# Optimization experiments

Hardware: AMD Instinct MI355X
Metric: run time of the kernel (lower is better)

The kernel has to match this reference:

```python
import jax, jax.numpy as jnp
import numpy as np

D, N, L, H, VOCAB = 256, 8192, 6, 4, 256
EPS = 1e-5


def layernorm(x):
    # LayerNorm over last dim, no affine (matches nn.LayerNorm(D, elementwise_affine=False))
    mu = jnp.mean(x, axis=-1, keepdims=True)
    var = jnp.mean(jnp.square(x - mu), axis=-1, keepdims=True)
    return (x - mu) * jax.lax.rsqrt(var + EPS)


def rotate_half(x):
    x1, x2 = jnp.split(x, 2, axis=-1)
    return jnp.concatenate((-x2, x1), axis=-1)


def rope_tables(T, dim, dtype):
    inv_freq = 1.0 / (10000.0 ** (jnp.arange(0, dim, 2, dtype=jnp.float32) / dim))
    t = jnp.arange(T, dtype=jnp.float32)
    freqs = jnp.einsum('i,j->ij', t, inv_freq)          # [T, dim/2]
    emb = jnp.concatenate((freqs, freqs), axis=-1)       # [T, dim]
    return jnp.cos(emb).astype(dtype), jnp.sin(emb).astype(dtype)


def linear_attention(Q, K, V):
    # unnormalized causal attention with RoPE on Q, K
    B, T, d = Q.shape
    cos, sin = rope_tables(T, d, Q.dtype)
    Qr = Q * cos + rotate_half(Q) * sin
    Kr = K * cos + rotate_half(K) * sin
    energy = jnp.einsum('btd,bsd->bts', Qr, Kr)          # [B, T, T]
    mask = jnp.tril(jnp.ones((T, T), dtype=energy.dtype))
    energy = energy * mask
    return jnp.einsum('bts,bsd->btd', energy, V)


def setup_inputs() -> dict:
    key = jax.random.key(0)
    ks = jax.random.split(key, 6)
    idx = jax.random.randint(ks[0], (4, 2048), 0, VOCAB)
    wte = jax.random.normal(ks[1], (VOCAB, D), dtype=jnp.float32) * 0.02
    encoder = jax.random.normal(ks[2], (N, D), dtype=jnp.float32) * 0.02
    decoder_x = jax.random.normal(ks[3], (H, D, N // H), dtype=jnp.float32) * 0.02
    decoder_y = jax.random.normal(ks[4], (H, D, N // H), dtype=jnp.float32) * 0.02
    readout = jax.random.normal(ks[5], (D, VOCAB), dtype=jnp.float32) * 0.02
    return {"idx": idx, "wte": wte, "encoder": encoder,
            "decoder_x": decoder_x, "decoder_y": decoder_y, "readout": readout}


def reference(idx, wte, encoder, decoder_x, decoder_y, readout):
    B, T = idx.shape
    v_ast = layernorm(wte[idx])                          # [B, T, D]
    for _ in range(L):
        x_raw = jnp.einsum('btd,hdm->bthm', v_ast, decoder_x)
        x = jax.nn.relu(x_raw)                           # [B, T, H, N/H]
        a_ast = linear_attention(v_ast, v_ast, v_ast)
        y_raw = jnp.einsum('btd,hdm->bthm', layernorm(a_ast), decoder_y)
        y = jax.nn.relu(y_raw) * x
        y_flat = y.reshape(B, T, -1)                     # [B, T, N]
        update = y_flat @ encoder                        # [B, T, D]
        v_ast = v_ast + layernorm(update)
    logits = v_ast @ readout                             # [B, T, VOCAB]
    return logits
```

## Files before the change

kernel.cpp:

```cpp
#include <hip/hip_runtime.h>
#include <hip/hip_bf16.h>

typedef __hip_bfloat16 bf16;
typedef _Float16 half_t;
typedef __attribute__((ext_vector_type(8))) _Float16 half8;
typedef __attribute__((ext_vector_type(4))) float f32x4;

#define LN_EPS 1e-5f

static constexpr int Dk     = 256;
static constexpr int Tk     = 2048;
static constexpr int BTk    = 8192;
static constexpr int MHk    = 2048;
static constexpr int Nk     = 8192;
static constexpr int LAYERS = 6;
static constexpr long long TD  = (long long)Tk * Dk;
static constexpr long long BTD = (long long)BTk * Dk;
static constexpr long long TT  = (long long)Tk * Tk;

#define SKQ(t) ((((t) & 3) ^ (((t) >> 3) & 3)) * 8)

__device__ __forceinline__ float wave_reduce(float v) {
#pragma unroll
    for (int o = 32; o > 0; o >>= 1) v += __shfl_down(v, o);
    return v;
}

__device__ __forceinline__ float block_sum_256(float x, float* sbuf) {
    float s = wave_reduce(x);
    int lane = threadIdx.x & 63, wv = threadIdx.x >> 6;
    if (lane == 0) sbuf[wv] = s;
    __syncthreads();
    float r = sbuf[0] + sbuf[1] + sbuf[2] + sbuf[3];
    __syncthreads();
    return r;
}

__device__ __forceinline__ void glds16(const void* g, void* lds) {
    __builtin_amdgcn_global_load_lds(
        (const __attribute__((address_space(1))) void*)g,
        (__attribute__((address_space(3))) void*)lds, 16, 0, 0);
}

__device__ __forceinline__ void rope_row(const float* nv, int t, half_t* qrow) {
    int i = threadIdx.x;
    if (i < 128) {
        float invf = powf(10000.f, -(float)i / 128.f);
        float ang = (float)t * invf;
        float s, c;
        sincosf(ang, &s, &c);
        float q1 = nv[i], q2 = nv[128 + i];
        qrow[i]       = (half_t)(q1 * c - q2 * s);
        qrow[128 + i] = (half_t)(q2 * c + q1 * s);
    }
}

__global__ __launch_bounds__(256) void sniff_kernel(const unsigned short* __restrict__ w,
                                                    int* __restrict__ flag) {
    __shared__ float sbuf[4];
    int tid = threadIdx.x;
    float cnt = 0.f;
    for (int i = tid; i < 1024; i += 256) {
        int e = (w[i] >> 7) & 0xFF;
        if (e >= 128) cnt += 1.f;
    }
    float tot = block_sum_256(cnt, sbuf);
    if (tid == 0) *flag = (tot > 32.f) ? 1 : 0;
}

__global__ __launch_bounds__(256) void tr_cvt16_kernel(const void* __restrict__ src,
                                                       const int* __restrict__ flag,
                                                       half_t* __restrict__ dst,
                                                       int R, int C,
                                                       long long sz, long long dz) {
    __shared__ float t[32][33];
    bool f32 = (*flag != 0);
    int ct = blockIdx.x * 32, rt = blockIdx.y * 32;
    long long so = (long long)blockIdx.z * sz, dofs = (long long)blockIdx.z * dz;
    int tx = threadIdx.x & 31, ty = threadIdx.x >> 5;
#pragma unroll
    for (int i = 0; i < 4; i++) {
        long long idx = so + (long long)(rt + ty + i * 8) * C + ct + tx;
        t[ty + i * 8][tx] = f32 ? ((const float*)src)[idx] : (float)((const bf16*)src)[idx];
    }
    __syncthreads();
#pragma unroll
    for (int i = 0; i < 4; i++) {
        long long odx = dofs + (long long)(ct + ty + i * 8) * R + rt + tx;
        dst[odx] = (half_t)t[tx][ty + i * 8];
    }
}

__global__ __launch_bounds__(256) void trv_kernel(const float* __restrict__ src,
                                                  half_t* __restrict__ dst) {
    __shared__ float t[32][33];
    int ct = blockIdx.x * 32, rt = blockIdx.y * 32;
    int tx = threadIdx.x & 31, ty = threadIdx.x >> 5;
#pragma unroll
    for (int i = 0; i < 4; i++)
        t[ty + i * 8][tx] = src[(long long)(rt + ty + i * 8) * Dk + ct + tx];
    __syncthreads();
#pragma unroll
    for (int i = 0; i < 4; i++)
        dst[(long long)(ct + ty + i * 8) * BTk + rt + tx] = (half_t)t[tx][ty + i * 8];
}

__global__ __launch_bounds__(256) void embed_ln_kernel(const int* __restrict__ idx,
                                                       const void* __restrict__ wte,
                                                       const int* __restrict__ flag,
                                                       float* __restrict__ v,
                                                       half_t* __restrict__ vf,
                                                       half_t* __restrict__ qf) {
    __shared__ float sbuf[4];
    __shared__ float nvs[256];
    int bt = blockIdx.x, tid = threadIdx.x;
    int id = idx[bt];
    bool f32 = (*flag != 0);
    float x = f32 ? ((const float*)wte)[id * Dk + tid]
                  : (float)((const bf16*)wte)[id * Dk + tid];
    float mu = block_sum_256(x, sbuf) * (1.f / 256.f);
    float d = x - mu;
    float var = block_sum_256(d * d, sbuf) * (1.f / 256.f);
    float r = d * rsqrtf(var + LN_EPS);
    v[bt * Dk + tid] = r;
    vf[bt * Dk + tid] = (half_t)r;
    nvs[tid] = r;
    __syncthreads();
    rope_row(nvs, bt & (Tk - 1), qf + (long long)bt * Dk);
}

__global__ __launch_bounds__(256) void ln_rows_kernel(const float* __restrict__ Pa,
                                                      half_t* __restrict__ of) {
    __shared__ float sbuf[4];
    int bt = blockIdx.x, tid = threadIdx.x;
    int b = bt >> 11, t = bt & (Tk - 1);
    int ncnt = ((t & ~127) >> 9) + 1;
    const float* p = Pa + ((long long)(b << 2)) * TD + (long long)t * Dk + tid;
    float x = 0.f;
    for (int c = 0; c < ncnt; c++) x += p[(long long)c * TD];
    float mu = block_sum_256(x, sbuf) * (1.f / 256.f);
    float d = x - mu;
    float var = block_sum_256(d * d, sbuf) * (1.f / 256.f);
    float r = d * rsqrtf(var + LN_EPS);
    of[bt * Dk + tid] = (half_t)r;
}

__global__ __launch_bounds__(256) void add_ln_kernel(const float* __restrict__ Pu,
                                                     float* __restrict__ v,
                                                     half_t* __restrict__ vf,
                                                     half_t* __restrict__ qf) {
    __shared__ float sbuf[4];
    __shared__ float nvs[256];
    int bt = blockIdx.x, tid = threadIdx.x;
    long long e = (long long)bt * Dk + tid;
    float x = Pu[e] + Pu[e + BTD] + Pu[e + 2 * BTD] + Pu[e + 3 * BTD];
    float mu = block_sum_256(x, sbuf) * (1.f / 256.f);
    float d = x - mu;
    float var = block_sum_256(d * d, sbuf) * (1.f / 256.f);
    float r = d * rsqrtf(var + LN_EPS);
    float nv = v[e] + r;
    v[e] = nv;
    vf[e] = (half_t)nv;
    nvs[tid] = nv;
    __syncthreads();
    rope_row(nvs, bt & (Tk - 1), qf + (long long)bt * Dk);
}

__global__ __launch_bounds__(256) void gemm128e(
    const half_t* __restrict__ Q, half_t* __restrict__ E) {
    __shared__ __align__(16) half_t As[128 * 32];
    __shared__ __align__(16) half_t Bs[128 * 32];
    const int tid = threadIdx.x;
    const int lane = tid & 63, wv = tid >> 6;
    const int wr = wv >> 1, wc = wv & 1;
    const int quad = lane >> 4, r = lane & 15;
    const int qsw = (quad ^ ((r >> 1) & 3)) * 8;
    const int mb = blockIdx.y * 128, nb = blockIdx.x * 128;
    if ((int)blockIdx.x > (int)blockIdx.y) return;
    const half_t* Qb = Q + (long long)blockIdx.z * TD;
    half_t* Eb = E + (long long)blockIdx.z * TT;

    f32x4 acc[4][4] = {};
    const int srow = tid >> 2, skq = SKQ(tid);
    const int wbase = (tid & 192) * 8;
    for (int k0 = 0; k0 < Dk; k0 += 32) {
#pragma unroll
        for (int rnd = 0; rnd < 2; rnd++) {
            int row = rnd * 64 + srow;
            glds16(Qb + (long long)(mb + row) * Dk + k0 + skq, As + rnd * 2048 + wbase);
            glds16(Qb + (long long)(nb + row) * Dk + k0 + skq, Bs + rnd * 2048 + wbase);
        }
        __syncthreads();
        half8 bfr[4];
#pragma unroll
        for (int ni = 0; ni < 4; ni++)
            bfr[ni] = *(const half8*)&Bs[(wc * 64 + ni * 16 + r) * 32 + qsw];
#pragma unroll
        for (int mi = 0; mi < 4; mi++) {
            half8 afr = *(const half8*)&As[(wr * 64 + mi * 16 + r) * 32 + qsw];
#pragma unroll
            for (int ni = 0; ni < 4; ni++)
                acc[mi][ni] = __builtin_amdgcn_mfma_f32_16x16x32_f16(afr, bfr[ni], acc[mi][ni], 0, 0, 0);
        }
        __syncthreads();
    }
#pragma unroll
    for (int mi = 0; mi < 4; mi++)
#pragma unroll
        for (int ni = 0; ni < 4; ni++) {
            int row0 = mb + wr * 64 + mi * 16 + quad * 4;
            int col = nb + wc * 64 + ni * 16 + r;
#pragma unroll
            for (int rr = 0; rr < 4; rr++) {
                int row = row0 + rr;
                float val = (row < col) ? 0.f : acc[mi][ni][rr];
                Eb[(long long)row * Tk + col] = (half_t)val;
            }
        }
}

__global__ __launch_bounds__(256) void gemm128a(
    const half_t* __restrict__ E, const half_t* __restrict__ vT,
    float* __restrict__ Pa) {
    __shared__ __align__(16) half_t As[128 * 32];
    __shared__ __align__(16) half_t Bs[128 * 32];
    const int tid = threadIdx.x;
    const int lane = tid & 63, wv = tid >> 6;
    const int wr = wv >> 1, wc = wv & 1;
    const int quad = lane >> 4, r = lane & 15;
    const int qsw = (quad ^ ((r >> 1) & 3)) * 8;
    const int mb = blockIdx.x * 128, nb = blockIdx.y * 128;
    const int b = blockIdx.z >> 2, c = blockIdx.z & 3;
    const int kbeg = c * 512;
    const int kend = min(mb + 128, kbeg + 512);
    if (kend <= kbeg) return;

    const half_t* Ab = E + (long long)b * TT;
    const half_t* Bb = vT + (long long)b * Tk;
    float* Pc = Pa + (long long)blockIdx.z * TD;
    f32x4 acc[4][4] = {};
    const int srow = tid >> 2, skq = SKQ(tid);
    const int wbase = (tid & 192) * 8;
    for (int k0 = kbeg; k0 < kend; k0 += 32) {
#pragma unroll
        for (int rnd = 0; rnd < 2; rnd++) {
            int row = rnd * 64 + srow;
            glds16(Ab + (long long)(mb + row) * Tk + k0 + skq, As + rnd * 2048 + wbase);
            glds16(Bb + (long long)(nb + row) * BTk + k0 + skq, Bs + rnd * 2048 + wbase);
        }
        __syncthreads();
        half8 bfr[4];
#pragma unroll
        for (int ni = 0; ni < 4; ni++)
            bfr[ni] = *(const half8*)&Bs[(wc * 64 + ni * 16 + r) * 32 + qsw];
#pragma unroll
        for (int mi = 0; mi < 4; mi++) {
            half8 afr = *(const half8*)&As[(wr * 64 + mi * 16 + r) * 32 + qsw];
#pragma unroll
            for (int ni = 0; ni < 4; ni++)
                acc[mi][ni] = __builtin_amdgcn_mfma_f32_16x16x32_f16(afr, bfr[ni], acc[mi][ni], 0, 0, 0);
        }
        __syncthreads();
    }
#pragma unroll
    for (int mi = 0; mi < 4; mi++)
#pragma unroll
        for (int ni = 0; ni < 4; ni++) {
            int row0 = mb + wr * 64 + mi * 16 + quad * 4;
            int col = nb + wc * 64 + ni * 16 + r;
#pragma unroll
            for (int rr = 0; rr < 4; rr++)
                Pc[(long long)(row0 + rr) * Dk + col] = acc[mi][ni][rr];
        }
}

__global__ __launch_bounds__(256, 2) void dual_gemm(
    const half_t* __restrict__ A1,
    const half_t* __restrict__ A2,
    const half_t* __restrict__ dxT,
    const half_t* __restrict__ dyT,
    half_t* __restrict__ C) {
    __shared__ __align__(16) half_t As1[128 * 64];
    __shared__ __align__(16) half_t As2[128 * 64];
    __shared__ __align__(16) half_t Bs1[128 * 64];
    __shared__ __align__(16) half_t Bs2[128 * 64];
    const int tid = threadIdx.x;
    const int lane = tid & 63, wv = tid >> 6;
    const int wr = wv >> 1, wc = wv & 1;
    const int quad = lane >> 4, r = lane & 15;
    const int flat = blockIdx.x + 16 * (blockIdx.y + 64 * blockIdx.z);
    const int xcd = flat & 7, j = flat >> 3;
    const int mt = (xcd >> 2) * 32 + (j >> 4);
    const int nt = (xcd & 3) * 4 + (j & 3);
    const int h  = (j >> 2) & 3;
    const int mb = mt * 128, nb = nt * 128;
    const half_t* B1 = dxT + (long long)h * MHk * Dk;
    const half_t* B2 = dyT + (long long)h * MHk * Dk;

    f32x4 accX[4][4] = {};
    f32x4 accY[4][4] = {};
    const int srow8 = lane >> 3;
    const int soct  = (lane & 7) ^ srow8;
    for (int k0 = 0; k0 < Dk; k0 += 64) {
#pragma unroll
        for (int c = 0; c < 4; c++) {
            int row = wv * 32 + c * 8;
            long long ga = (long long)(mb + row + srow8) * Dk + k0 + soct * 8;
            long long gb = (long long)(nb + row + srow8) * Dk + k0 + soct * 8;
            glds16(A1 + ga, As1 + row * 64);
            glds16(A2 + ga, As2 + row * 64);
            glds16(B1 + gb, Bs1 + row * 64);
            glds16(B2 + gb, Bs2 + row * 64);
        }
        __syncthreads();
#pragma unroll
        for (int sub = 0; sub < 2; sub++) {
            half8 b1f[4], b2f[4];
#pragma unroll
            for (int ni = 0; ni < 4; ni++) {
                int R = wc * 64 + ni * 16 + r;
                int pos = ((sub * 4 + quad) ^ (R & 7)) * 8;
                b1f[ni] = *(const half8*)&Bs1[R * 64 + pos];
                b2f[ni] = *(const half8*)&Bs2[R * 64 + pos];
            }
#pragma unroll
            for (int mi = 0; mi < 4; mi++) {
                int R = wr * 64 + mi * 16 + r;
                int pos = ((sub * 4 + quad) ^ (R & 7)) * 8;
                half8 a1 = *(const half8*)&As1[R * 64 + pos];
                half8 a2 = *(const half8*)&As2[R * 64 + pos];
#pragma unroll
                for (int ni = 0; ni < 4; ni++) {
                    accX[mi][ni] = __builtin_amdgcn_mfma_f32_16x16x32_f16(a1, b1f[ni], accX[mi][ni], 0, 0, 0);
                    accY[mi][ni] = __builtin_amdgcn_mfma_f32_16x16x32_f16(a2, b2f[ni], accY[mi][ni], 0, 0, 0);
                }
            }
        }
        __syncthreads();
    }
#pragma unroll
    for (int mi = 0; mi < 4; mi++)
#pragma unroll
        for (int ni = 0; ni < 4; ni++) {
            int row0 = mb + wr * 64 + mi * 16 + quad * 4;
            int col = h * MHk + nb + wc * 64 + ni * 16 + r;
#pragma unroll
            for (int rr = 0; rr < 4; rr++) {
                float val = fmaxf(accY[mi][ni][rr], 0.f) * fmaxf(accX[mi][ni][rr], 0.f);
                C[(long long)(row0 + rr) * Nk + col] = (half_t)val;
            }
        }
}

__global__ __launch_bounds__(256) void gemm128u(
    const half_t* __restrict__ A, const half_t* __restrict__ B,
    float* __restrict__ Pu) {
    __shared__ __align__(16) half_t As[128 * 32];
    __shared__ __align__(16) half_t Bs[128 * 32];
    const int tid = threadIdx.x;
    const int lane = tid & 63, wv = tid >> 6;
    const int wr = wv >> 1, wc = wv & 1;
    const int quad = lane >> 4, r = lane & 15;
    const int qsw = (quad ^ ((r >> 1) & 3)) * 8;
    const int mb = blockIdx.x * 128, nb = blockIdx.y * 128;
    const int kbeg = blockIdx.z * 2048;
    float* Pc = Pu + (long long)blockIdx.z * BTD;

    f32x4 acc[4][4] = {};
    const int srow = tid >> 2, skq = SKQ(tid);
    const int wbase = (tid & 192) * 8;
    for (int k0 = kbeg; k0 < kbeg + 2048; k0 += 32) {
#pragma unroll
        for (int rnd = 0; rnd < 2; rnd++) {
            int row = rnd * 64 + srow;
            glds16(A + (long long)(mb + row) * Nk + k0 + skq, As + rnd * 2048 + wbase);
            glds16(B + (long long)(nb + row) * Nk + k0 + skq, Bs + rnd * 2048 + wbase);
        }
        __syncthreads();
        half8 bfr[4];
#pragma unroll
        for (int ni = 0; ni < 4; ni++)
            bfr[ni] = *(const half8*)&Bs[(wc * 64 + ni * 16 + r) * 32 + qsw];
#pragma unroll
        for (int mi = 0; mi < 4; mi++) {
            half8 afr = *(const half8*)&As[(wr * 64 + mi * 16 + r) * 32 + qsw];
#pragma unroll
            for (int ni = 0; ni < 4; ni++)
                acc[mi][ni] = __builtin_amdgcn_mfma_f32_16x16x32_f16(afr, bfr[ni], acc[mi][ni], 0, 0, 0);
        }
        __syncthreads();
    }
#pragma unroll
    for (int mi = 0; mi < 4; mi++)
#pragma unroll
        for (int ni = 0; ni < 4; ni++) {
            int row0 = mb + wr * 64 + mi * 16 + quad * 4;
            int col = nb + wc * 64 + ni * 16 + r;
#pragma unroll
            for (int rr = 0; rr < 4; rr++)
                Pc[(long long)(row0 + rr) * Dk + col] = acc[mi][ni][rr];
        }
}

__global__ __launch_bounds__(256) void gemm64h(
    const half_t* __restrict__ A, int lda,
    const half_t* __restrict__ B, int ldb,
    float* __restrict__ C, int ldc, int K) {
    __shared__ __align__(16) half_t As[64 * 32];
    __shared__ __align__(16) half_t Bs[64 * 32];
    const int tid = threadIdx.x;
    const int lane = tid & 63, wv = tid >> 6;
    const int wr = wv >> 1, wc = wv & 1;
    const int quad = lane >> 4, r = lane & 15;
    const int qsw = (quad ^ ((r >> 1) & 3)) * 8;
    const int mb = blockIdx.y * 64, nb = blockIdx.x * 64;

    f32x4 acc[2][2] = {};
    const int srow = tid >> 2, skq = SKQ(tid);
    const int wbase = (tid & 192) * 8;
    for (int k0 = 0; k0 < K; k0 += 32) {
        glds16(A + (long long)(mb + srow) * lda + k0 + skq, As + wbase);
        glds16(B + (long long)(nb + srow) * ldb + k0 + skq, Bs + wbase);
        __syncthreads();
        half8 b0 = *(const half8*)&Bs[(wc * 32 +  0 + r) * 32 + qsw];
        half8 b1 = *(const half8*)&Bs[(wc * 32 + 16 + r) * 32 + qsw];
#pragma unroll
        for (int mi = 0; mi < 2; mi++) {
            half8 afr = *(const half8*)&As[(wr * 32 + mi * 16 + r) * 32 + qsw];
            acc[mi][0] = __builtin_amdgcn_mfma_f32_16x16x32_f16(afr, b0, acc[mi][0], 0, 0, 0);
            acc[mi][1] = __builtin_amdgcn_mfma_f32_16x16x32_f16(afr, b1, acc[mi][1], 0, 0, 0);
        }
        __syncthreads();
    }
#pragma unroll
    for (int mi = 0; mi < 2; mi++)
#pragma unroll
        for (int ni = 0; ni < 2; ni++) {
            int row0 = mb + wr * 32 + mi * 16 + quad * 4;
            int col = nb + wc * 32 + ni * 16 + r;
#pragma unroll
            for (int rr = 0; rr < 4; rr++)
                C[(long long)(row0 + rr) * ldc + col] = acc[mi][ni][rr];
        }
}

extern "C" void kernel_launch(void* const* d_in, const int* in_sizes, int n_in,
                              void* d_out, int out_size, void* d_ws, size_t ws_size,
                              hipStream_t stream) {
    (void)in_sizes; (void)n_in; (void)out_size; (void)ws_size;
    const int* idx = (const int*)d_in[0];
    float* out = (float*)d_out;

    char* ws = (char*)d_ws;
    float*  v32  = (float*) (ws);
    half_t* vf   = (half_t*)(ws + (  8ll << 20));
    half_t* qf   = (half_t*)(ws + ( 12ll << 20));
    half_t* vT   = (half_t*)(ws + ( 16ll << 20));
    half_t* lnf  = (half_t*)(ws + ( 20ll << 20));
    half_t* E    = (half_t*)(ws + ( 24ll << 20));
    float*  Pa   = (float*) (ws + ( 56ll << 20));
    float*  Pu   = (float*) (ws + ( 24ll << 20));
    half_t* y16  = (half_t*)(ws + ( 88ll << 20));
    half_t* dxT  = (half_t*)(ws + (216ll << 20));
    half_t* dyT  = (half_t*)(ws + (220ll << 20));
    half_t* eT   = (half_t*)(ws + (224ll << 20));
    half_t* roT  = (half_t*)(ws + (228ll << 20));
    int*    flag = (int*)   (ws + (228ll << 20) + (256ll << 10));

    sniff_kernel<<<1, 256, 0, stream>>>((const unsigned short*)d_in[1], flag);
    tr_cvt16_kernel<<<dim3(MHk / 32, Dk / 32, 4), 256, 0, stream>>>(
        d_in[3], flag, dxT, Dk, MHk, (long long)Dk * MHk, (long long)Dk * MHk);
    tr_cvt16_kernel<<<dim3(MHk / 32, Dk / 32, 4), 256, 0, stream>>>(
        d_in[4], flag, dyT, Dk, MHk, (long long)Dk * MHk, (long long)Dk * MHk);
    tr_cvt16_kernel<<<dim3(Dk / 32, Nk / 32, 1), 256, 0, stream>>>(
        d_in[2], flag, eT, Nk, Dk, 0, 0);
    tr_cvt16_kernel<<<dim3(Dk / 32, Dk / 32, 1), 256, 0, stream>>>(
        d_in[5], flag, roT, Dk, Dk, 0, 0);

    embed_ln_kernel<<<BTk, 256, 0, stream>>>(idx, d_in[1], flag, v32, vf, qf);

    for (int l = 0; l < LAYERS; l++) {
        trv_kernel<<<dim3(Dk / 32, BTk / 32), 256, 0, stream>>>(v32, vT);
        gemm128e<<<dim3(Tk / 128, Tk / 128, 4), 256, 0, stream>>>(qf, E);
        gemm128a<<<dim3(Tk / 128, Dk / 128, 16), 256, 0, stream>>>(E, vT, Pa);
        ln_rows_kernel<<<BTk, 256, 0, stream>>>(Pa, lnf);
        dual_gemm<<<dim3(MHk / 128, BTk / 128, 4), 256, 0, stream>>>(
            vf, lnf, dxT, dyT, y16);
        gemm128u<<<dim3(BTk / 128, Dk / 128, 4), 256, 0, stream>>>(y16, eT, Pu);
        add_ln_kernel<<<BTk, 256, 0, stream>>>(Pu, v32, vf, qf);
    }
    gemm64h<<<dim3(Dk / 64, BTk / 64), 256, 0, stream>>>(
        vf, Dk, roT, Dk, out, Dk, Dk);
}
```

Measured before the change: 1.281 ms.

## Fuse dual decoder GEMM with encoder GEMM, keeping y tiles in LDS

Merges the dual decoder GEMM (relu(x)*relu(y)) and the encoder projection into one kernel. Each block owns 128 rows and one head and loops over 16 column tiles of that head. Each y tile is written to LDS and immediately multiplied against the matching slice of the encoder, accumulating into a 128x256 register tile. This removes the round trip of the 8192x8192 fp16 y intermediate through global memory and drops one launch. In exchange there are only 256 blocks at occupancy 1, more accumulator registers per thread and serialized phases, so latency hiding and parallelism may suffer.

```diff
diff --git a/kernel.cpp b/kernel.cpp
--- a/kernel.cpp
+++ b/kernel.cpp
@@ -274,131 +274,135 @@
         }
 }
 
-__global__ __launch_bounds__(256, 2) void dual_gemm(
+__global__ __launch_bounds__(256, 1) void dual_update(
     const half_t* __restrict__ A1,
     const half_t* __restrict__ A2,
     const half_t* __restrict__ dxT,
     const half_t* __restrict__ dyT,
-    half_t* __restrict__ C) {
-    __shared__ __align__(16) half_t As1[128 * 64];
-    __shared__ __align__(16) half_t As2[128 * 64];
-    __shared__ __align__(16) half_t Bs1[128 * 64];
-    __shared__ __align__(16) half_t Bs2[128 * 64];
-    const int tid = threadIdx.x;
-    const int lane = tid & 63, wv = tid >> 6;
-    const int wr = wv >> 1, wc = wv & 1;
-    const int quad = lane >> 4, r = lane & 15;
-    const int flat = blockIdx.x + 16 * (blockIdx.y + 64 * blockIdx.z);
-    const int xcd = flat & 7, j = flat >> 3;
-    const int mt = (xcd >> 2) * 32 + (j >> 4);
-    const int nt = (xcd & 3) * 4 + (j & 3);
-    const int h  = (j >> 2) & 3;
-    const int mb = mt * 128, nb = nt * 128;
-    const half_t* B1 = dxT + (long long)h * MHk * Dk;
-    const half_t* B2 = dyT + (long long)h * MHk * Dk;
-
-    f32x4 accX[4][4] = {};
-    f32x4 accY[4][4] = {};
-    const int srow8 = lane >> 3;
-    const int soct  = (lane & 7) ^ srow8;
-    for (int k0 = 0; k0 < Dk; k0 += 64) {
-#pragma unroll
-        for (int c = 0; c < 4; c++) {
-            int row = wv * 32 + c * 8;
-            long long ga = (long long)(mb + row + srow8) * Dk + k0 + soct * 8;
-            long long gb = (long long)(nb + row + srow8) * Dk + k0 + soct * 8;
-            glds16(A1 + ga, As1 + row * 64);
-            glds16(A2 + ga, As2 + row * 64);
-            glds16(B1 + gb, Bs1 + row * 64);
-            glds16(B2 + gb, Bs2 + row * 64);
-        }
-        __syncthreads();
-#pragma unroll
-        for (int sub = 0; sub < 2; sub++) {
-            half8 b1f[4], b2f[4];
-#pragma unroll
-            for (int ni = 0; ni < 4; ni++) {
-                int R = wc * 64 + ni * 16 + r;
-                int pos = ((sub * 4 + quad) ^ (R & 7)) * 8;
-                b1f[ni] = *(const half8*)&Bs1[R * 64 + pos];
-                b2f[ni] = *(const half8*)&Bs2[R * 64 + pos];
-            }
-#pragma unroll
-            for (int mi = 0; mi < 4; mi++) {
-                int R = wr * 64 + mi * 16 + r;
-                int pos = ((sub * 4 + quad) ^ (R & 7)) * 8;
-                half8 a1 = *(const half8*)&As1[R * 64 + pos];
-                half8 a2 = *(const half8*)&As2[R * 64 + pos];
-#pragma unroll
-                for (int ni = 0; ni < 4; ni++) {
-                    accX[mi][ni] = __builtin_amdgcn_mfma_f32_16x16x32_f16(a1, b1f[ni], accX[mi][ni], 0, 0, 0);
-                    accY[mi][ni] = __builtin_amdgcn_mfma_f32_16x16x32_f16(a2, b2f[ni], accY[mi][ni], 0, 0, 0);
-                }
-            }
-        }
-        __syncthreads();
-    }
-#pragma unroll
-    for (int mi = 0; mi < 4; mi++)
-#pragma unroll
-        for (int ni = 0; ni < 4; ni++) {
-            int row0 = mb + wr * 64 + mi * 16 + quad * 4;
-            int col = h * MHk + nb + wc * 64 + ni * 16 + r;
-#pragma unroll
-            for (int rr = 0; rr < 4; rr++) {
-                float val = fmaxf(accY[mi][ni][rr], 0.f) * fmaxf(accX[mi][ni][rr], 0.f);
-                C[(long long)(row0 + rr) * Nk + col] = (half_t)val;
-            }
-        }
-}
-
-__global__ __launch_bounds__(256) void gemm128u(
-    const half_t* __restrict__ A, const half_t* __restrict__ B,
+    const half_t* __restrict__ eT,
     float* __restrict__ Pu) {
-    __shared__ __align__(16) half_t As[128 * 32];
-    __shared__ __align__(16) half_t Bs[128 * 32];
+    __shared__ __align__(16) half_t smem[32768];
+    half_t* As1 = smem;
+    half_t* As2 = smem + 8192;
+    half_t* Bs1 = smem + 16384;
+    half_t* Bs2 = smem + 24576;
+    half_t* yld = smem;
+    half_t* eTs = smem + 16384;
+
     const int tid = threadIdx.x;
     const int lane = tid & 63, wv = tid >> 6;
     const int wr = wv >> 1, wc = wv & 1;
     const int quad = lane >> 4, r = lane & 15;
     const int qsw = (quad ^ ((r >> 1) & 3)) * 8;
-    const int mb = blockIdx.x * 128, nb = blockIdx.y * 128;
-    const int kbeg = blockIdx.z * 2048;
-    float* Pc = Pu + (long long)blockIdx.z * BTD;
-
-    f32x4 acc[4][4] = {};
+    const int xcd = blockIdx.x & 7, j = blockIdx.x >> 3;
+    const int mt = xcd * 8 + (j & 7);
+    const int h = j >> 3;
+    const int mb = mt * 128;
+    const half_t* B1 = dxT + (long long)h * MHk * Dk;
+    const half_t* B2 = dyT + (long long)h * MHk * Dk;
+    const half_t* Eh = eT + (long long)h * MHk;
+    float* Pc = Pu + (long long)h * BTD;
+
+    const int srow8 = lane >> 3;
+    const int soct  = (lane & 7) ^ srow8;
     const int srow = tid >> 2, skq = SKQ(tid);
     const int wbase = (tid & 192) * 8;
-    for (int k0 = kbeg; k0 < kbeg + 2048; k0 += 32) {
-#pragma unroll
-        for (int rnd = 0; rnd < 2; rnd++) {
+
+    f32x4 accU[4][8] = {};
+    for (int nt = 0; nt < 16; ++nt) {
+        const int nb = nt * 128;
+        f32x4 accX[4][4] = {};
+        f32x4 accY[4][4] = {};
+        for (int k0 = 0; k0 < Dk; k0 += 64) {
+#pragma unroll
+            for (int st = 0; st < 4; st++) {
+                int row = wv * 32 + st * 8;
+                long long ga = (long long)(mb + row + srow8) * Dk + k0 + soct * 8;
+                long long gb = (long long)(nb + row + srow8) * Dk + k0 + soct * 8;
+                glds16(A1 + ga, As1 + row * 64);
+                glds16(A2 + ga, As2 + row * 64);
+                glds16(B1 + gb, Bs1 + row * 64);
+                glds16(B2 + gb, Bs2 + row * 64);
+            }
+            __syncthreads();
+#pragma unroll
+            for (int sub = 0; sub < 2; sub++) {
+                half8 b1f[4], b2f[4];
+#pragma unroll
+                for (int ni = 0; ni < 4; ni++) {
+                    int R = wc * 64 + ni * 16 + r;
+                    int pos = ((sub * 4 + quad) ^ (R & 7)) * 8;
+                    b1f[ni] = *(const half8*)&Bs1[R * 64 + pos];
+                    b2f[ni] = *(const half8*)&Bs2[R * 64 + pos];
+                }
+#pragma unroll
+                for (int mi = 0; mi < 4; mi++) {
+                    int R = wr * 64 + mi * 16 + r;
+                    int pos = ((sub * 4 + quad) ^ (R & 7)) * 8;
+                    half8 a1 = *(const half8*)&As1[R * 64 + pos];
+                    half8 a2 = *(const half8*)&As2[R * 64 + pos];
+#pragma unroll
+                    for (int ni = 0; ni < 4; ni++) {
+                        accX[mi][ni] = __builtin_amdgcn_mfma_f32_16x16x32_f16(a1, b1f[ni], accX[mi][ni], 0, 0, 0);
+                        accY[mi][ni] = __builtin_amdgcn_mfma_f32_16x16x32_f16(a2, b2f[ni], accY[mi][ni], 0, 0, 0);
+                    }
+                }
+            }
+            __syncthreads();
+        }
+#pragma unroll
+        for (int mi = 0; mi < 4; mi++)
+#pragma unroll
+            for (int ni = 0; ni < 4; ni++) {
+                int col = wc * 64 + ni * 16 + r;
+                int row0 = wr * 64 + mi * 16 + quad * 4;
+#pragma unroll
+                for (int rr = 0; rr < 4; rr++) {
+                    int W = row0 + rr;
+                    float val = fmaxf(accY[mi][ni][rr], 0.f) * fmaxf(accX[mi][ni][rr], 0.f);
+                    yld[W * 128 + (((col >> 3) ^ ((W & 12) >> 1)) << 3) + (col & 7)] = (half_t)val;
+                }
+            }
+#pragma unroll
+        for (int rnd = 0; rnd < 4; rnd++) {
             int row = rnd * 64 + srow;
-            glds16(A + (long long)(mb + row) * Nk + k0 + skq, As + rnd * 2048 + wbase);
-            glds16(B + (long long)(nb + row) * Nk + k0 + skq, Bs + rnd * 2048 + wbase);
-        }
-        __syncthreads();
-        half8 bfr[4];
-#pragma unroll
-        for (int ni = 0; ni < 4; ni++)
-            bfr[ni] = *(const half8*)&Bs[(wc * 64 + ni * 16 + r) * 32 + qsw];
-#pragma unroll
-        for (int mi = 0; mi < 4; mi++) {
-            half8 afr = *(const half8*)&As[(wr * 64 + mi * 16 + r) * 32 + qsw];
-#pragma unroll
-            for (int ni = 0; ni < 4; ni++)
-                acc[mi][ni] = __builtin_amdgcn_mfma_f32_16x16x32_f16(afr, bfr[ni], acc[mi][ni], 0, 0, 0);
-        }
-        __syncthreads();
+            glds16(Eh + (long long)row * Nk + nb + skq, eTs + rnd * 2048 + wbase);
+        }
+        __syncthreads();
+#pragma unroll
+        for (int c = 0; c < 4; ++c) {
+            if (c < 3) {
+#pragma unroll
+                for (int rnd = 0; rnd < 4; rnd++) {
+                    int row = rnd * 64 + srow;
+                    glds16(Eh + (long long)row * Nk + nb + (c + 1) * 32 + skq,
+                           eTs + ((c + 1) & 1) * 8192 + rnd * 2048 + wbase);
+                }
+            }
+            half8 bu[8];
+#pragma unroll
+            for (int ni = 0; ni < 8; ni++)
+                bu[ni] = *(const half8*)&eTs[(c & 1) * 8192 + (wc * 128 + ni * 16 + r) * 32 + qsw];
+#pragma unroll
+            for (int mi = 0; mi < 4; mi++) {
+                int R = wr * 64 + mi * 16 + r;
+                half8 au = *(const half8*)&yld[R * 128 + ((((c << 2) + quad) ^ ((R & 12) >> 1)) << 3)];
+#pragma unroll
+                for (int ni = 0; ni < 8; ni++)
+                    accU[mi][ni] = __builtin_amdgcn_mfma_f32_16x16x32_f16(au, bu[ni], accU[mi][ni], 0, 0, 0);
+            }
+            __syncthreads();
+        }
     }
 #pragma unroll
     for (int mi = 0; mi < 4; mi++)
 #pragma unroll
-        for (int ni = 0; ni < 4; ni++) {
+        for (int ni = 0; ni < 8; ni++) {
             int row0 = mb + wr * 64 + mi * 16 + quad * 4;
-            int col = nb + wc * 64 + ni * 16 + r;
+            int col = wc * 128 + ni * 16 + r;
 #pragma unroll
             for (int rr = 0; rr < 4; rr++)
-                Pc[(long long)(row0 + rr) * Dk + col] = acc[mi][ni][rr];
+                Pc[(long long)(row0 + rr) * Dk + col] = accU[mi][ni][rr];
         }
 }
 
@@ -460,7 +464,6 @@
     half_t* E    = (half_t*)(ws + ( 24ll << 20));
     float*  Pa   = (float*) (ws + ( 56ll << 20));
     float*  Pu   = (float*) (ws + ( 24ll << 20));
-    half_t* y16  = (half_t*)(ws + ( 88ll << 20));
     half_t* dxT  = (half_t*)(ws + (216ll << 20));
     half_t* dyT  = (half_t*)(ws + (220ll << 20));
     half_t* eT   = (half_t*)(ws + (224ll << 20));
@@ -484,9 +487,7 @@
         gemm128e<<<dim3(Tk / 128, Tk / 128, 4), 256, 0, stream>>>(qf, E);
         gemm128a<<<dim3(Tk / 128, Dk / 128, 16), 256, 0, stream>>>(E, vT, Pa);
         ln_rows_kernel<<<BTk, 256, 0, stream>>>(Pa, lnf);
-        dual_gemm<<<dim3(MHk / 128, BTk / 128, 4), 256, 0, stream>>>(
-            vf, lnf, dxT, dyT, y16);
-        gemm128u<<<dim3(BTk / 128, Dk / 128, 4), 256, 0, stream>>>(y16, eT, Pu);
+        dual_update<<<dim3(256), 256, 0, stream>>>(vf, lnf, dxT, dyT, eT, Pu);
         add_ln_kernel<<<BTk, 256, 0, stream>>>(Pu, v32, vf, qf);
     }
     gemm64h<<<dim3(Dk / 64, BTk / 64), 256, 0, stream>>>(
```

New measurement: 1.527 ms. +19.2%, slower.

## Double-buffer LDS staging in dual_gemm and gemm128u with wave priority boost

Applied to the files above, without the earlier changes.

Both the dual projection GEMM and the split-K encoder GEMM now use two LDS buffers. The global-to-LDS loads for the next K step are issued before the MFMA work on the current buffer, so each iteration needs one barrier instead of two. dual_gemm also switches from a 64-wide K tile to a 32-wide one so the double buffer fits in the same LDS budget. MFMA sections are wrapped in s_setprio, and gemm128u gets a launch bound of 2 blocks per CU. The cost is more barriers in dual_gemm (8 K steps instead of 4) and doubled LDS use in gemm128u, which could limit occupancy.

```diff
diff --git a/kernel.cpp b/kernel.cpp
--- a/kernel.cpp
+++ b/kernel.cpp
@@ -280,14 +280,15 @@
     const half_t* __restrict__ dxT,
     const half_t* __restrict__ dyT,
     half_t* __restrict__ C) {
-    __shared__ __align__(16) half_t As1[128 * 64];
-    __shared__ __align__(16) half_t As2[128 * 64];
-    __shared__ __align__(16) half_t Bs1[128 * 64];
-    __shared__ __align__(16) half_t Bs2[128 * 64];
+    __shared__ __align__(16) half_t As1[2][128 * 32];
+    __shared__ __align__(16) half_t As2[2][128 * 32];
+    __shared__ __align__(16) half_t Bs1[2][128 * 32];
+    __shared__ __align__(16) half_t Bs2[2][128 * 32];
     const int tid = threadIdx.x;
     const int lane = tid & 63, wv = tid >> 6;
     const int wr = wv >> 1, wc = wv & 1;
     const int quad = lane >> 4, r = lane & 15;
+    const int qsw = (quad ^ ((r >> 1) & 3)) * 8;
     const int flat = blockIdx.x + 16 * (blockIdx.y + 64 * blockIdx.z);
     const int xcd = flat & 7, j = flat >> 3;
     const int mt = (xcd >> 2) * 32 + (j >> 4);
@@ -299,43 +300,48 @@
 
     f32x4 accX[4][4] = {};
     f32x4 accY[4][4] = {};
-    const int srow8 = lane >> 3;
-    const int soct  = (lane & 7) ^ srow8;
-    for (int k0 = 0; k0 < Dk; k0 += 64) {
-#pragma unroll
-        for (int c = 0; c < 4; c++) {
-            int row = wv * 32 + c * 8;
-            long long ga = (long long)(mb + row + srow8) * Dk + k0 + soct * 8;
-            long long gb = (long long)(nb + row + srow8) * Dk + k0 + soct * 8;
-            glds16(A1 + ga, As1 + row * 64);
-            glds16(A2 + ga, As2 + row * 64);
-            glds16(B1 + gb, Bs1 + row * 64);
-            glds16(B2 + gb, Bs2 + row * 64);
-        }
-        __syncthreads();
-#pragma unroll
-        for (int sub = 0; sub < 2; sub++) {
-            half8 b1f[4], b2f[4];
+    const int srow = tid >> 2, skq = SKQ(tid);
+    const int wbase = (tid & 192) * 8;
+
+    auto stage = [&](int ks, int bsel) {
+        const int k0 = ks * 32;
+#pragma unroll
+        for (int rnd = 0; rnd < 2; rnd++) {
+            int row = rnd * 64 + srow;
+            long long ga = (long long)(mb + row) * Dk + k0 + skq;
+            long long gb = (long long)(nb + row) * Dk + k0 + skq;
+            glds16(A1 + ga, &As1[bsel][rnd * 2048 + wbase]);
+            glds16(A2 + ga, &As2[bsel][rnd * 2048 + wbase]);
+            glds16(B1 + gb, &Bs1[bsel][rnd * 2048 + wbase]);
+            glds16(B2 + gb, &Bs2[bsel][rnd * 2048 + wbase]);
+        }
+    };
+
+    stage(0, 0);
+    __syncthreads();
+    for (int ks = 0; ks < 8; ks++) {
+        const int cur = ks & 1;
+        if (ks < 7) stage(ks + 1, cur ^ 1);
+        __builtin_amdgcn_s_setprio(1);
+        half8 b1f[4], b2f[4];
+#pragma unroll
+        for (int ni = 0; ni < 4; ni++) {
+            int R = wc * 64 + ni * 16 + r;
+            b1f[ni] = *(const half8*)&Bs1[cur][R * 32 + qsw];
+            b2f[ni] = *(const half8*)&Bs2[cur][R * 32 + qsw];
+        }
+#pragma unroll
+        for (int mi = 0; mi < 4; mi++) {
+            int R = wr * 64 + mi * 16 + r;
+            half8 a1 = *(const half8*)&As1[cur][R * 32 + qsw];
+            half8 a2 = *(const half8*)&As2[cur][R * 32 + qsw];
 #pragma unroll
             for (int ni = 0; ni < 4; ni++) {
-                int R = wc * 64 + ni * 16 + r;
-                int pos = ((sub * 4 + quad) ^ (R & 7)) * 8;
-                b1f[ni] = *(const half8*)&Bs1[R * 64 + pos];
-                b2f[ni] = *(const half8*)&Bs2[R * 64 + pos];
+                accX[mi][ni] = __builtin_amdgcn_mfma_f32_16x16x32_f16(a1, b1f[ni], accX[mi][ni], 0, 0, 0);
+                accY[mi][ni] = __builtin_amdgcn_mfma_f32_16x16x32_f16(a2, b2f[ni], accY[mi][ni], 0, 0, 0);
             }
-#pragma unroll
-            for (int mi = 0; mi < 4; mi++) {
-                int R = wr * 64 + mi * 16 + r;
-                int pos = ((sub * 4 + quad) ^ (R & 7)) * 8;
-                half8 a1 = *(const half8*)&As1[R * 64 + pos];
-                half8 a2 = *(const half8*)&As2[R * 64 + pos];
-#pragma unroll
-                for (int ni = 0; ni < 4; ni++) {
-                    accX[mi][ni] = __builtin_amdgcn_mfma_f32_16x16x32_f16(a1, b1f[ni], accX[mi][ni], 0, 0, 0);
-                    accY[mi][ni] = __builtin_amdgcn_mfma_f32_16x16x32_f16(a2, b2f[ni], accY[mi][ni], 0, 0, 0);
-                }
-            }
-        }
+        }
+        __builtin_amdgcn_s_setprio(0);
         __syncthreads();
     }
 #pragma unroll
@@ -352,11 +358,11 @@
         }
 }
 
-__global__ __launch_bounds__(256) void gemm128u(
+__global__ __launch_bounds__(256, 2) void gemm128u(
     const half_t* __restrict__ A, const half_t* __restrict__ B,
     float* __restrict__ Pu) {
-    __shared__ __align__(16) half_t As[128 * 32];
-    __shared__ __align__(16) half_t Bs[128 * 32];
+    __shared__ __align__(16) half_t As[2][128 * 32];
+    __shared__ __align__(16) half_t Bs[2][128 * 32];
     const int tid = threadIdx.x;
     const int lane = tid & 63, wv = tid >> 6;
     const int wr = wv >> 1, wc = wv & 1;
@@ -369,25 +375,34 @@
     f32x4 acc[4][4] = {};
     const int srow = tid >> 2, skq = SKQ(tid);
     const int wbase = (tid & 192) * 8;
-    for (int k0 = kbeg; k0 < kbeg + 2048; k0 += 32) {
+
+    auto stage = [&](int k0, int bsel) {
 #pragma unroll
         for (int rnd = 0; rnd < 2; rnd++) {
             int row = rnd * 64 + srow;
-            glds16(A + (long long)(mb + row) * Nk + k0 + skq, As + rnd * 2048 + wbase);
-            glds16(B + (long long)(nb + row) * Nk + k0 + skq, Bs + rnd * 2048 + wbase);
-        }
-        __syncthreads();
+            glds16(A + (long long)(mb + row) * Nk + k0 + skq, &As[bsel][rnd * 2048 + wbase]);
+            glds16(B + (long long)(nb + row) * Nk + k0 + skq, &Bs[bsel][rnd * 2048 + wbase]);
+        }
+    };
+
+    stage(kbeg, 0);
+    __syncthreads();
+    for (int ks = 0; ks < 64; ks++) {
+        const int cur = ks & 1;
+        if (ks < 63) stage(kbeg + (ks + 1) * 32, cur ^ 1);
+        __builtin_amdgcn_s_setprio(1);
         half8 bfr[4];
 #pragma unroll
         for (int ni = 0; ni < 4; ni++)
-            bfr[ni] = *(const half8*)&Bs[(wc * 64 + ni * 16 + r) * 32 + qsw];
+            bfr[ni] = *(const half8*)&Bs[cur][(wc * 64 + ni * 16 + r) * 32 + qsw];
 #pragma unroll
         for (int mi = 0; mi < 4; mi++) {
-            half8 afr = *(const half8*)&As[(wr * 64 + mi * 16 + r) * 32 + qsw];
+            half8 afr = *(const half8*)&As[cur][(wr * 64 + mi * 16 + r) * 32 + qsw];
 #pragma unroll
             for (int ni = 0; ni < 4; ni++)
                 acc[mi][ni] = __builtin_amdgcn_mfma_f32_16x16x32_f16(afr, bfr[ni], acc[mi][ni], 0, 0, 0);
         }
+        __builtin_amdgcn_s_setprio(0);
         __syncthreads();
     }
 #pragma unroll
```

Measured after the change: 1.336 ms. 1.04x slower.

## Pipeline encoder GEMM with 4-stage LDS ring and XCD-aware block mapping

Applied to the files above, without the earlier changes.

Rewrites the update GEMM (y @ encoder) so that it prefetches three K-tiles ahead into a four-buffer LDS ring. It uses explicit vmcnt waits and a single barrier per step instead of two __syncthreads, and raises wave priority during the MFMA section. The grid is flattened to 1D and remapped so that blocks on the same XCD share M rows, with the two N tiles and K-split placed nearby, to improve L2 reuse. The larger LDS footprint (64KB) and the launch_bounds occupancy hint change occupancy. The hand-tuned waitcnt counts depend on the glds16 issue count per stage.

```diff
diff --git a/kernel.cpp b/kernel.cpp
--- a/kernel.cpp
+++ b/kernel.cpp
@@ -352,44 +352,76 @@
         }
 }
 
-__global__ __launch_bounds__(256) void gemm128u(
+__global__ __launch_bounds__(256, 2) void gemm128u(
     const half_t* __restrict__ A, const half_t* __restrict__ B,
     float* __restrict__ Pu) {
-    __shared__ __align__(16) half_t As[128 * 32];
-    __shared__ __align__(16) half_t Bs[128 * 32];
+    __shared__ __align__(16) half_t As[4][128 * 32];
+    __shared__ __align__(16) half_t Bs[4][128 * 32];
     const int tid = threadIdx.x;
     const int lane = tid & 63, wv = tid >> 6;
     const int wr = wv >> 1, wc = wv & 1;
     const int quad = lane >> 4, r = lane & 15;
     const int qsw = (quad ^ ((r >> 1) & 3)) * 8;
-    const int mb = blockIdx.x * 128, nb = blockIdx.y * 128;
-    const int kbeg = blockIdx.z * 2048;
-    float* Pc = Pu + (long long)blockIdx.z * BTD;
+    const int flat = blockIdx.x;
+    const int xcd = flat & 7, j = flat >> 3;
+    const int nb = (j & 1) * 128;
+    const int kc = (j >> 1) & 3;
+    const int mb = (xcd * 8 + (j >> 3)) * 128;
+    const int kbeg = kc * 2048;
+    float* Pc = Pu + (long long)kc * BTD;
 
     f32x4 acc[4][4] = {};
     const int srow = tid >> 2, skq = SKQ(tid);
     const int wbase = (tid & 192) * 8;
-    for (int k0 = kbeg; k0 < kbeg + 2048; k0 += 32) {
+
+    auto stage = [&](int ks) {
+        const int k0 = kbeg + ks * 32;
+        const int bsel = ks & 3;
 #pragma unroll
         for (int rnd = 0; rnd < 2; rnd++) {
             int row = rnd * 64 + srow;
-            glds16(A + (long long)(mb + row) * Nk + k0 + skq, As + rnd * 2048 + wbase);
-            glds16(B + (long long)(nb + row) * Nk + k0 + skq, Bs + rnd * 2048 + wbase);
-        }
-        __syncthreads();
+            glds16(A + (long long)(mb + row) * Nk + k0 + skq, &As[bsel][rnd * 2048 + wbase]);
+            glds16(B + (long long)(nb + row) * Nk + k0 + skq, &Bs[bsel][rnd * 2048 + wbase]);
+        }
+    };
+    auto compute = [&](int ks) {
+        const int cur = ks & 3;
         half8 bfr[4];
 #pragma unroll
         for (int ni = 0; ni < 4; ni++)
-            bfr[ni] = *(const half8*)&Bs[(wc * 64 + ni * 16 + r) * 32 + qsw];
+            bfr[ni] = *(const half8*)&Bs[cur][(wc * 64 + ni * 16 + r) * 32 + qsw];
 #pragma unroll
         for (int mi = 0; mi < 4; mi++) {
-            half8 afr = *(const half8*)&As[(wr * 64 + mi * 16 + r) * 32 + qsw];
+            half8 afr = *(const half8*)&As[cur][(wr * 64 + mi * 16 + r) * 32 + qsw];
 #pragma unroll
             for (int ni = 0; ni < 4; ni++)
                 acc[mi][ni] = __builtin_amdgcn_mfma_f32_16x16x32_f16(afr, bfr[ni], acc[mi][ni], 0, 0, 0);
         }
-        __syncthreads();
-    }
+    };
+
+    stage(0); stage(1); stage(2);
+    for (int ks = 0; ks < 61; ks++) {
+        asm volatile("s_waitcnt vmcnt(8)" ::: "memory");
+        __builtin_amdgcn_s_barrier();
+        __builtin_amdgcn_sched_barrier(0);
+        stage(ks + 3);
+        __builtin_amdgcn_s_setprio(1);
+        compute(ks);
+        __builtin_amdgcn_s_setprio(0);
+    }
+    asm volatile("s_waitcnt vmcnt(8)" ::: "memory");
+    __builtin_amdgcn_s_barrier();
+    __builtin_amdgcn_sched_barrier(0);
+    compute(61);
+    asm volatile("s_waitcnt vmcnt(4)" ::: "memory");
+    __builtin_amdgcn_s_barrier();
+    __builtin_amdgcn_sched_barrier(0);
+    compute(62);
+    asm volatile("s_waitcnt vmcnt(0)" ::: "memory");
+    __builtin_amdgcn_s_barrier();
+    __builtin_amdgcn_sched_barrier(0);
+    compute(63);
+
 #pragma unroll
     for (int mi = 0; mi < 4; mi++)
 #pragma unroll
@@ -486,7 +518,7 @@
         ln_rows_kernel<<<BTk, 256, 0, stream>>>(Pa, lnf);
         dual_gemm<<<dim3(MHk / 128, BTk / 128, 4), 256, 0, stream>>>(
             vf, lnf, dxT, dyT, y16);
-        gemm128u<<<dim3(BTk / 128, Dk / 128, 4), 256, 0, stream>>>(y16, eT, Pu);
+        gemm128u<<<dim3(512), 256, 0, stream>>>(y16, eT, Pu);
         add_ln_kernel<<<BTk, 256, 0, stream>>>(Pu, v32, vf, qf);
     }
     gemm64h<<<dim3(Dk / 64, BTk / 64), 256, 0, stream>>>(
```

Measured after the change: 1.250 ms (median of 3 runs). 2.4% less time.
